# Optimization experiments

Measured on AMD Instinct MI355X. Metric: run time of the kernel, lower is better.

## Reference

```python
import jax, jax.numpy as jnp
import numpy as np

ALPHA = 0.2  # LeakyReLU negative slope
NEG = -1e12


def setup_inputs() -> dict:
    key = jax.random.key(0)
    ks = jax.random.split(key, 7)
    B, N, Cin, F, H = 4, 2048, 256, 64, 4
    x = jax.random.normal(ks[0], (B, N, Cin), dtype=jnp.float32)
    adj = jax.random.randint(ks[1], (N, N), 0, 2, dtype=jnp.int32)
    W = jax.random.normal(ks[2], (H, Cin, F), dtype=jnp.float32) * (1.414 / np.sqrt(Cin))
    a1 = jax.random.normal(ks[3], (H, F), dtype=jnp.float32) * 0.1
    a2 = jax.random.normal(ks[4], (H, F), dtype=jnp.float32) * 0.1
    Wl = jax.random.normal(ks[5], (F, H * F), dtype=jnp.float32) * (1.0 / np.sqrt(H * F))
    bl = jax.random.normal(ks[6], (F,), dtype=jnp.float32) * 0.01
    return {"x": x, "adj": adj, "W": W, "a1": a1, "a2": a2, "Wl": Wl, "bl": bl}


def leaky(v):
    return jnp.where(v >= 0, v, ALPHA * v)


def reference(x, adj, W, a1, a2, Wl, bl):
    # Eval mode: dropout is a no-op.
    # h: [B,H,N,F] per-head projected features
    h = jnp.einsum("bnc,hcf->bhnf", x, W)
    # additive attention: e[b,h,i,j] = leaky(h_i . a1 + h_j . a2)
    f1 = jnp.einsum("bhnf,hf->bhn", h, a1)  # source term
    f2 = jnp.einsum("bhnf,hf->bhn", h, a2)  # target term
    e = leaky(f1[:, :, :, None] + f2[:, :, None, :])  # [B,H,N,N]
    e = jnp.where(adj[None, None] > 0, e, NEG)
    # NOTE: original softmaxes over dim=1 of [B,N,N], i.e. the i axis (axis=2 here)
    att = jax.nn.softmax(e, axis=2)
    hp = jnp.einsum("bhij,bhjf->bhif", att, h)  # [B,H,N,F]
    hp = jax.nn.relu(hp)  # concat=True heads
    B, H, N, F = hp.shape
    cat = hp.transpose(0, 2, 1, 3).reshape(B, N, H * F)
    out = leaky(cat @ Wl.T + bl)  # n_heads > 1 -> linear + leakyrelu
    return out
```

## Files before the change

kernel.cpp:

```cpp
#include <hip/hip_runtime.h>
#include <hip/hip_bf16.h>
#include <stdint.h>

typedef __attribute__((ext_vector_type(8))) short short8;
typedef __attribute__((ext_vector_type(4))) float f32x4;
typedef uint32_t u32;
typedef uint16_t u16;
typedef uint8_t u8;

#define LOG2E 1.4426950408889634f


__device__ __forceinline__ u16 f2bf(float f){
  union{float f; u32 u;} x; x.f = f;
  u32 r = x.u + 0x7FFFu + ((x.u >> 16) & 1u);
  return (u16)(r >> 16);
}
__device__ __forceinline__ u32 pkbf(float a, float b){
  __hip_bfloat162 h = __float22bfloat162_rn(float2{a, b});
  union{ __hip_bfloat162 h; u32 u; } cv; cv.h = h;
  return cv.u;
}
__device__ __forceinline__ float bflo(u32 cd){ union{u32 u; float f;} v; v.u = cd << 16; return v.f; }
__device__ __forceinline__ float bfhi(u32 cd){ union{u32 u; float f;} v; v.u = cd & 0xFFFF0000u; return v.f; }

__global__ __launch_bounds__(256) void k_front(const float* __restrict__ x,
      const float* __restrict__ W, const float* __restrict__ a1, const float* __restrict__ a2,
      const int* __restrict__ adj,
      u8* __restrict__ adjb, u16* __restrict__ hT,
      float* __restrict__ Aarr, float* __restrict__ Barr,
      float* __restrict__ Cexp, float* __restrict__ Dexp,
      float* __restrict__ Dsum){
  int bid = blockIdx.x, t = threadIdx.x;

  if (bid >= 2560){
    Dsum[(bid - 2560)*256 + t] = 0.f;
    return;
  }
  if (bid >= 512){
    int idx = (bid - 512)*256 + t;
    const int4* ap = (const int4*)(adj + (size_t)idx*8);
    int4 v0 = ap[0], v1 = ap[1];
    u32 byte = (u32)(v0.x > 0)        | ((u32)(v0.y > 0) << 1)
             | ((u32)(v0.z > 0) << 2) | ((u32)(v0.w > 0) << 3)
             | ((u32)(v1.x > 0) << 4) | ((u32)(v1.y > 0) << 5)
             | ((u32)(v1.z > 0) << 6) | ((u32)(v1.w > 0) << 7);
    adjb[idx] = (u8)byte;
    return;
  }
  __shared__ u16 WL[64*264];
  int rt = bid & 127, cb = bid >> 7;
  const float* Wh = W + (size_t)cb*16384;
  #pragma unroll 4
  for (int p = 0; p < 16; p++){
    int idx = p*256 + t;
    float4 wv = ((const float4*)Wh)[idx];
    int off = idx*4; int c = off >> 6, f0 = off & 63;
    int cc = c ^ (((f0 >> 2) & 7) << 3);
    WL[(f0+0)*264 + cc] = f2bf(wv.x);
    WL[(f0+1)*264 + cc] = f2bf(wv.y);
    WL[(f0+2)*264 + cc] = f2bf(wv.z);
    WL[(f0+3)*264 + cc] = f2bf(wv.w);
  }
  __syncthreads();

  int w = t >> 6, l = t & 63;
  int rA = rt*64 + w*16 + (l & 15);
  int kg = (l >> 4) * 8;
  int rowq[4], rswq[4];
  #pragma unroll
  for (int q = 0; q < 4; q++){
    rowq[q] = q*16 + (l & 15);
    rswq[q] = ((rowq[q] >> 2) & 7) << 3;
  }
  f32x4 acc[4] = {};
  const float* xrow = x + (size_t)rA * 256;
  #pragma unroll
  for (int ks = 0; ks < 8; ks++){
    int c = ks*32 + kg;
    float4 xa = *(const float4*)(xrow + c);
    float4 xb = *(const float4*)(xrow + c + 4);
    union{u32 w[4]; short8 v;} A;
    A.w[0] = pkbf(xa.x, xa.y); A.w[1] = pkbf(xa.z, xa.w);
    A.w[2] = pkbf(xb.x, xb.y); A.w[3] = pkbf(xb.z, xb.w);
    #pragma unroll
    for (int q = 0; q < 4; q++){
      short8 Bf = *(const short8*)&WL[rowq[q]*264 + (c ^ rswq[q])];
      acc[q] = __builtin_amdgcn_mfma_f32_16x16x32_bf16(A.v, Bf, acc[q], 0, 0, 0);
    }
  }
  int rb = rt*64 + w*16 + (l >> 4)*4;
  int b = rb >> 11, n = rb & 2047;
  #pragma unroll
  for (int q = 0; q < 4; q++){
    int f = q*16 + (l & 15);
    u32 p0 = pkbf(acc[q][0], acc[q][1]);
    u32 p1 = pkbf(acc[q][2], acc[q][3]);
    u16* dst = hT + ((size_t)(b*4 + cb)*64 + f)*2048 + n;
    *(uint2*)dst = uint2{p0, p1};
  }
  float a1v[4], a2v[4];
  #pragma unroll
  for (int q = 0; q < 4; q++){
    a1v[q] = a1[cb*64 + q*16 + (l & 15)];
    a2v[q] = a2[cb*64 + q*16 + (l & 15)];
  }
  float s1[4], s2[4];
  #pragma unroll
  for (int r = 0; r < 4; r++){
    s1[r] = acc[0][r]*a1v[0] + acc[1][r]*a1v[1] + acc[2][r]*a1v[2] + acc[3][r]*a1v[3];
    s2[r] = acc[0][r]*a2v[0] + acc[1][r]*a2v[1] + acc[2][r]*a2v[2] + acc[3][r]*a2v[3];
  }
  #pragma unroll
  for (int m = 1; m <= 8; m <<= 1){
    #pragma unroll
    for (int r = 0; r < 4; r++){
      s1[r] += __shfl_xor(s1[r], m);
      s2[r] += __shfl_xor(s2[r], m);
    }
  }
  if ((l & 15) == 0){
    #pragma unroll
    for (int r = 0; r < 4; r++){
      int row = rb + r;
      int bb = row >> 11, nn = row & 2047;
      int o = (bb*4 + cb)*2048 + nn;
      float fa = s1[r] * LOG2E;
      Aarr[o] = __builtin_amdgcn_exp2f(fa);
      Barr[o] = __builtin_amdgcn_exp2f(0.2f*fa);
      float fb = s2[r] * LOG2E;
      Cexp[o] = __builtin_amdgcn_exp2f(fb);
      Dexp[o] = __builtin_amdgcn_exp2f(0.2f*fb);
    }
  }
}

__global__ __launch_bounds__(256) void k_colsum(const u32* __restrict__ adjw,
      const float* __restrict__ Aarr, const float* __restrict__ Barr,
      const float* __restrict__ Cexp, const float* __restrict__ Dexp,
      float* __restrict__ Dsum){
  __shared__ float AL[128*16], BL[128*16];
  __shared__ float red[4][1024];
  int jt = blockIdx.x;
  int is = blockIdx.y;
  int t = threadIdx.x, w = t >> 6, l = t & 63;
  int i0 = is*128;
  for (int k = t; k < 2048; k += 256){
    int bh = k >> 7, ii = k & 127;
    AL[ii*16 + bh] = Aarr[bh*2048 + i0 + ii];
    BL[ii*16 + bh] = Barr[bh*2048 + i0 + ii];
  }
  int j = jt*64 + l;
  float Cj[16], Dj[16];
  #pragma unroll
  for (int bh = 0; bh < 16; bh++){
    Cj[bh] = Cexp[bh*2048 + j];
    Dj[bh] = Dexp[bh*2048 + j];
  }
  float acc[16] = {};
  __syncthreads();
  int wi = jt*2 + (l >> 5), sh = l & 31;
  const u32* aw = adjw + wi;
  #pragma unroll 2
  for (int ii = w*32; ii < w*32 + 32; ii++){
    u32 m = aw[(size_t)(i0 + ii)*64];
    float bitf = (float)((m >> sh) & 1u);
    const float* ar = &AL[ii*16];
    const float* br = &BL[ii*16];
    #pragma unroll
    for (int q = 0; q < 4; q++){
      float4 a4 = *(const float4*)(ar + q*4);
      float4 b4 = *(const float4*)(br + q*4);
      acc[q*4+0] = fmaf(fmaxf(a4.x*Cj[q*4+0], b4.x*Dj[q*4+0]), bitf, acc[q*4+0]);
      acc[q*4+1] = fmaf(fmaxf(a4.y*Cj[q*4+1], b4.y*Dj[q*4+1]), bitf, acc[q*4+1]);
      acc[q*4+2] = fmaf(fmaxf(a4.z*Cj[q*4+2], b4.z*Dj[q*4+2]), bitf, acc[q*4+2]);
      acc[q*4+3] = fmaf(fmaxf(a4.w*Cj[q*4+3], b4.w*Dj[q*4+3]), bitf, acc[q*4+3]);
    }
  }
  #pragma unroll
  for (int bh = 0; bh < 16; bh++) red[w][bh*64 + l] = acc[bh];
  __syncthreads();
  #pragma unroll
  for (int k = 0; k < 4; k++){
    int e = t*4 + k;
    float s = (red[0][e] + red[1][e]) + (red[2][e] + red[3][e]);
    int bh = e >> 6, jl = e & 63;
    atomicAdd(&Dsum[bh*2048 + jt*64 + jl], s);
  }
}

__global__ __launch_bounds__(256) void k_pv(const u32* __restrict__ adjw, const u16* __restrict__ hT,
      const float* __restrict__ Aarr, const float* __restrict__ Barr,
      const float* __restrict__ Cexp, const float* __restrict__ Dexp,
      const float* __restrict__ Dsum, u16* __restrict__ part){
  int it = blockIdx.x;
  int bh = blockIdx.y;
  int jh = blockIdx.z;
  int b = bh >> 2, h = bh & 3;
  int t = threadIdx.x;
  int w = t >> 6, l = t & 63;

  __shared__ u16 hTl[64*136];
  __shared__ u32 CDl[1024];

  {
    int gj = bh*2048 + jh*1024 + t*4;
    float4 c4 = *(const float4*)(Cexp + gj);
    float4 d4 = *(const float4*)(Dexp + gj);
    float4 s4 = *(const float4*)(Dsum + gj);
    float i0v = 1.0f/s4.x, i1v = 1.0f/s4.y, i2v = 1.0f/s4.z, i3v = 1.0f/s4.w;
    uint4 pk;
    pk.x = pkbf(c4.x*i0v, d4.x*i0v);
    pk.y = pkbf(c4.y*i1v, d4.y*i1v);
    pk.z = pkbf(c4.z*i2v, d4.z*i2v);
    pk.w = pkbf(c4.w*i3v, d4.w*i3v);
    *(uint4*)&CDl[t*4] = pk;
  }

  int i0 = it*128 + w*32 + (l & 15);
  float Ai0 = Aarr[bh*2048 + i0],      Bi0 = Barr[bh*2048 + i0];
  float Ai1 = Aarr[bh*2048 + i0 + 16], Bi1 = Barr[bh*2048 + i0 + 16];
  const u16* hTr = hT + (size_t)bh * 64 * 2048;
  int kg = (l >> 4) * 8;
  f32x4 acc[2][4] = {};

  for (int jj = 0; jj < 1024; jj += 128){
    int jc = jh*1024 + jj;
    __syncthreads();
    {
      int f = t >> 2, seg = (t & 3) * 32;
      const u16* src = hTr + (size_t)f*2048 + jc + seg;
      u16* d = hTl + f*136 + seg;
      *(uint4*)(d)      = *(const uint4*)(src);
      *(uint4*)(d + 8)  = *(const uint4*)(src + 8);
      *(uint4*)(d + 16) = *(const uint4*)(src + 16);
      *(uint4*)(d + 24) = *(const uint4*)(src + 24);
    }
    __syncthreads();
    uint4 mw0 = *(const uint4*)(adjw + (size_t)i0*64 + (jc >> 5));
    uint4 mw1 = *(const uint4*)(adjw + (size_t)(i0+16)*64 + (jc >> 5));
    #pragma unroll
    for (int ks = 0; ks < 4; ks++){
      u32 cd[8];
      *(uint4*)(cd)     = *(const uint4*)&CDl[jj + ks*32 + kg];
      *(uint4*)(cd + 4) = *(const uint4*)&CDl[jj + ks*32 + kg + 4];
      u32 w0 = (&mw0.x)[ks] >> kg;
      u32 w1 = (&mw1.x)[ks] >> kg;
      float wv0[8], wv1[8];
      #pragma unroll
      for (int e = 0; e < 8; e++){
        float ca = bflo(cd[e]), db = bfhi(cd[e]);
        float ev0 = fmaxf(Ai0*ca, Bi0*db);
        float ev1 = fmaxf(Ai1*ca, Bi1*db);
        wv0[e] = ((int)(w0 << (31-e)) < 0) ? ev0 : 0.f;
        wv1[e] = ((int)(w1 << (31-e)) < 0) ? ev1 : 0.f;
      }
      union{u32 w[4]; short8 v;} A0, A1;
      A0.w[0] = pkbf(wv0[0], wv0[1]); A0.w[1] = pkbf(wv0[2], wv0[3]);
      A0.w[2] = pkbf(wv0[4], wv0[5]); A0.w[3] = pkbf(wv0[6], wv0[7]);
      A1.w[0] = pkbf(wv1[0], wv1[1]); A1.w[1] = pkbf(wv1[2], wv1[3]);
      A1.w[2] = pkbf(wv1[4], wv1[5]); A1.w[3] = pkbf(wv1[6], wv1[7]);
      #pragma unroll
      for (int q = 0; q < 4; q++){
        short8 Bf = *(const short8*)&hTl[(q*16 + (l & 15))*136 + ks*32 + kg];
        acc[0][q] = __builtin_amdgcn_mfma_f32_16x16x32_bf16(A0.v, Bf, acc[0][q], 0, 0, 0);
        acc[1][q] = __builtin_amdgcn_mfma_f32_16x16x32_bf16(A1.v, Bf, acc[1][q], 0, 0, 0);
      }
    }
  }
  u16* pr = part + ((size_t)(jh*4 + b)*2048)*256;
  #pragma unroll
  for (int r = 0; r < 2; r++){
    int nb = it*128 + w*32 + r*16 + (l >> 4)*4;
    #pragma unroll
    for (int q = 0; q < 4; q++){
      int f = h*64 + q*16 + (l & 15);
      #pragma unroll
      for (int rr = 0; rr < 4; rr++){
        pr[(size_t)(nb + rr)*256 + f] = f2bf(acc[r][q][rr]);
      }
    }
  }
}

__global__ __launch_bounds__(256) void k_out(const u16* __restrict__ part,
                       const float* __restrict__ Wl, const float* __restrict__ bl,
                       float* __restrict__ out){
  int rt = blockIdx.x;
  int w = threadIdx.x >> 6, l = threadIdx.x & 63;
  int rA = rt*64 + w*16 + (l & 15);
  int b = rA >> 11, n = rA & 2047;
  const u16* p0 = part + ((size_t)b*2048 + n)*256;
  const u16* p1 = part + ((size_t)(4 + b)*2048 + n)*256;
  int kg = (l >> 4) * 8;
  f32x4 acc[4] = {};
  #pragma unroll
  for (int ks = 0; ks < 8; ks++){
    int c = ks*32 + kg;
    short8 v0 = *(const short8*)(p0 + c);
    short8 v1 = *(const short8*)(p1 + c);
    float av[8];
    #pragma unroll
    for (int e = 0; e < 8; e++){
      union{u32 u; float f;} x0, x1;
      x0.u = ((u32)(u16)v0[e]) << 16;
      x1.u = ((u32)(u16)v1[e]) << 16;
      av[e] = fmaxf(x0.f + x1.f, 0.f);
    }
    union{u32 w[4]; short8 v;} A;
    A.w[0] = pkbf(av[0], av[1]); A.w[1] = pkbf(av[2], av[3]);
    A.w[2] = pkbf(av[4], av[5]); A.w[3] = pkbf(av[6], av[7]);
    #pragma unroll
    for (int q = 0; q < 4; q++){
      const float* wr = Wl + (size_t)(q*16 + (l & 15))*256 + c;
      float4 u0 = *(const float4*)(wr);
      float4 u1 = *(const float4*)(wr + 4);
      union{u32 w[4]; short8 v;} Bv;
      Bv.w[0] = pkbf(u0.x, u0.y); Bv.w[1] = pkbf(u0.z, u0.w);
      Bv.w[2] = pkbf(u1.x, u1.y); Bv.w[3] = pkbf(u1.z, u1.w);
      acc[q] = __builtin_amdgcn_mfma_f32_16x16x32_bf16(A.v, Bv.v, acc[q], 0, 0, 0);
    }
  }
  int rb = rt*64 + w*16 + (l >> 4)*4;
  #pragma unroll
  for (int q = 0; q < 4; q++){
    int o = q*16 + (l & 15);
    float bv = bl[o];
    #pragma unroll
    for (int r = 0; r < 4; r++){
      float v = acc[q][r] + bv;
      out[(size_t)(rb + r)*64 + o] = fmaxf(v, 0.2f*v);
    }
  }
}

extern "C" void kernel_launch(void* const* d_in, const int* in_sizes, int n_in,
                              void* d_out, int out_size, void* d_ws, size_t ws_size,
                              hipStream_t stream) {
  const float* x  = (const float*)d_in[0];
  const int* adj  = (const int*)d_in[1];
  const float* W  = (const float*)d_in[2];
  const float* a1 = (const float*)d_in[3];
  const float* a2 = (const float*)d_in[4];
  const float* Wl = (const float*)d_in[5];
  const float* bl = (const float*)d_in[6];
  float* out = (float*)d_out;
  char* ws = (char*)d_ws;

  u32* adjw    = (u32*)(ws + 0x0000000);
  u16* hT      = (u16*)(ws + 0x0080000);
  u16* part    = (u16*)(ws + 0x0480000);
  float* Aarr  = (float*)(ws + 0x1480000);
  float* Barr  = (float*)(ws + 0x14A0000);
  float* Cexp  = (float*)(ws + 0x14C0000);
  float* Dexp  = (float*)(ws + 0x14E0000);
  float* Dsum  = (float*)(ws + 0x1500000);

  k_front<<<2688, 256, 0, stream>>>(x, W, a1, a2, adj, (u8*)adjw, hT, Aarr, Barr, Cexp, Dexp, Dsum);
  k_colsum<<<dim3(32, 16), 256, 0, stream>>>(adjw, Aarr, Barr, Cexp, Dexp, Dsum);
  k_pv<<<dim3(16, 16, 2), 256, 0, stream>>>(adjw, hT, Aarr, Barr, Cexp, Dexp, Dsum, part);
  k_out<<<128, 256, 0, stream>>>(part, Wl, bl, out);
}
```

Measured before the change: 71.31 us.

## Switch attention P·V path to packed fp16 math and fp16 MFMA

Stores the per-head projected features in fp16 instead of bf16. The P·V kernel now builds attention weights with packed half2 multiply/max and bitmask AND, replacing per-element fp32 math and bf16 packing, and feeds fp16 MFMA. Scale factors of 16 and 1/16 keep the values inside fp16 range. Separately, the W staging in the front kernel is rewritten to use coalesced row loads with packed 64-bit LDS stores. The trade is fewer VALU ops per weight against fp16 range and overflow risk for the exp-based terms.

```diff
diff --git a/kernel.cpp b/kernel.cpp
--- a/kernel.cpp
+++ b/kernel.cpp
@@ -4,6 +4,9 @@
 
 typedef __attribute__((ext_vector_type(8))) short short8;
 typedef __attribute__((ext_vector_type(4))) float f32x4;
+typedef _Float16 f16;
+typedef __attribute__((ext_vector_type(8))) f16 f16x8;
+typedef __attribute__((ext_vector_type(2))) f16 f16x2;
 typedef uint32_t u32;
 typedef uint16_t u16;
 typedef uint8_t u8;
@@ -21,8 +24,13 @@
   union{ __hip_bfloat162 h; u32 u; } cv; cv.h = h;
   return cv.u;
 }
-__device__ __forceinline__ float bflo(u32 cd){ union{u32 u; float f;} v; v.u = cd << 16; return v.f; }
-__device__ __forceinline__ float bfhi(u32 cd){ union{u32 u; float f;} v; v.u = cd & 0xFFFF0000u; return v.f; }
+__device__ __forceinline__ u32 pkh(float a, float b){
+  f16x2 h; h.x = (f16)a; h.y = (f16)b;
+  union{ f16x2 h; u32 u; } cv; cv.h = h;
+  return cv.u;
+}
+__device__ __forceinline__ f16x2 uh2(u32 x){ union{u32 u; f16x2 h;} v; v.u = x; return v.h; }
+__device__ __forceinline__ u32 h2u(f16x2 x){ union{f16x2 h; u32 u;} v; v.h = x; return v.u; }
 
 __global__ __launch_bounds__(256) void k_front(const float* __restrict__ x,
       const float* __restrict__ W, const float* __restrict__ a1, const float* __restrict__ a2,
@@ -51,16 +59,25 @@
   __shared__ u16 WL[64*264];
   int rt = bid & 127, cb = bid >> 7;
   const float* Wh = W + (size_t)cb*16384;
-  #pragma unroll 4
-  for (int p = 0; p < 16; p++){
-    int idx = p*256 + t;
-    float4 wv = ((const float4*)Wh)[idx];
-    int off = idx*4; int c = off >> 6, f0 = off & 63;
-    int cc = c ^ (((f0 >> 2) & 7) << 3);
-    WL[(f0+0)*264 + cc] = f2bf(wv.x);
-    WL[(f0+1)*264 + cc] = f2bf(wv.y);
-    WL[(f0+2)*264 + cc] = f2bf(wv.z);
-    WL[(f0+3)*264 + cc] = f2bf(wv.w);
+  {
+    int f0 = (t & 15)*4;
+    int cg = t >> 4;
+    int s = ((f0 >> 2) & 7) << 3;
+    #pragma unroll
+    for (int it2 = 0; it2 < 4; it2++){
+      int c0 = (cg + it2*16)*4;
+      float4 wv0 = *(const float4*)(Wh + (size_t)(c0+0)*64 + f0);
+      float4 wv1 = *(const float4*)(Wh + (size_t)(c0+1)*64 + f0);
+      float4 wv2 = *(const float4*)(Wh + (size_t)(c0+2)*64 + f0);
+      float4 wv3 = *(const float4*)(Wh + (size_t)(c0+3)*64 + f0);
+      int cc = c0 ^ s;
+      #pragma unroll
+      for (int k = 0; k < 4; k++){
+        u32 lo = pkbf((&wv0.x)[k], (&wv1.x)[k]);
+        u32 hi = pkbf((&wv2.x)[k], (&wv3.x)[k]);
+        *(uint2*)&WL[(f0+k)*264 + cc] = uint2{lo, hi};
+      }
+    }
   }
   __syncthreads();
 
@@ -94,8 +111,8 @@
   #pragma unroll
   for (int q = 0; q < 4; q++){
     int f = q*16 + (l & 15);
-    u32 p0 = pkbf(acc[q][0], acc[q][1]);
-    u32 p1 = pkbf(acc[q][2], acc[q][3]);
+    u32 p0 = pkh(acc[q][0], acc[q][1]);
+    u32 p1 = pkh(acc[q][2], acc[q][3]);
     u16* dst = hT + ((size_t)(b*4 + cb)*64 + f)*2048 + n;
     *(uint2*)dst = uint2{p0, p1};
   }
@@ -201,25 +218,30 @@
   int w = t >> 6, l = t & 63;
 
   __shared__ u16 hTl[64*136];
-  __shared__ u32 CDl[1024];
+  __shared__ u32 CA2l[512];
+  __shared__ u32 DB2l[512];
 
   {
     int gj = bh*2048 + jh*1024 + t*4;
     float4 c4 = *(const float4*)(Cexp + gj);
     float4 d4 = *(const float4*)(Dexp + gj);
     float4 s4 = *(const float4*)(Dsum + gj);
-    float i0v = 1.0f/s4.x, i1v = 1.0f/s4.y, i2v = 1.0f/s4.z, i3v = 1.0f/s4.w;
-    uint4 pk;
-    pk.x = pkbf(c4.x*i0v, d4.x*i0v);
-    pk.y = pkbf(c4.y*i1v, d4.y*i1v);
-    pk.z = pkbf(c4.z*i2v, d4.z*i2v);
-    pk.w = pkbf(c4.w*i3v, d4.w*i3v);
-    *(uint4*)&CDl[t*4] = pk;
+    float i0v = 16.0f/s4.x, i1v = 16.0f/s4.y, i2v = 16.0f/s4.z, i3v = 16.0f/s4.w;
+    CA2l[t*2]   = pkh(c4.x*i0v, c4.y*i1v);
+    CA2l[t*2+1] = pkh(c4.z*i2v, c4.w*i3v);
+    DB2l[t*2]   = pkh(d4.x*i0v, d4.y*i1v);
+    DB2l[t*2+1] = pkh(d4.z*i2v, d4.w*i3v);
   }
 
   int i0 = it*128 + w*32 + (l & 15);
-  float Ai0 = Aarr[bh*2048 + i0],      Bi0 = Barr[bh*2048 + i0];
-  float Ai1 = Aarr[bh*2048 + i0 + 16], Bi1 = Barr[bh*2048 + i0 + 16];
+  f16x2 Ai02, Bi02, Ai12, Bi12;
+  {
+    const float sc = 0.0625f;
+    float A0 = Aarr[bh*2048 + i0] * sc,      B0 = Barr[bh*2048 + i0] * sc;
+    float A1 = Aarr[bh*2048 + i0 + 16] * sc, B1 = Barr[bh*2048 + i0 + 16] * sc;
+    Ai02 = uh2(pkh(A0, A0)); Bi02 = uh2(pkh(B0, B0));
+    Ai12 = uh2(pkh(A1, A1)); Bi12 = uh2(pkh(B1, B1));
+  }
   const u16* hTr = hT + (size_t)bh * 64 * 2048;
   int kg = (l >> 4) * 8;
   f32x4 acc[2][4] = {};
@@ -241,30 +263,30 @@
     uint4 mw1 = *(const uint4*)(adjw + (size_t)(i0+16)*64 + (jc >> 5));
     #pragma unroll
     for (int ks = 0; ks < 4; ks++){
-      u32 cd[8];
-      *(uint4*)(cd)     = *(const uint4*)&CDl[jj + ks*32 + kg];
-      *(uint4*)(cd + 4) = *(const uint4*)&CDl[jj + ks*32 + kg + 4];
+      int pbase = (jj >> 1) + ks*16 + (l >> 4)*4;
+      uint4 ca2 = *(const uint4*)&CA2l[pbase];
+      uint4 db2 = *(const uint4*)&DB2l[pbase];
       u32 w0 = (&mw0.x)[ks] >> kg;
       u32 w1 = (&mw1.x)[ks] >> kg;
-      float wv0[8], wv1[8];
+      union{u32 w[4]; f16x8 v;} A0u, A1u;
       #pragma unroll
-      for (int e = 0; e < 8; e++){
-        float ca = bflo(cd[e]), db = bfhi(cd[e]);
-        float ev0 = fmaxf(Ai0*ca, Bi0*db);
-        float ev1 = fmaxf(Ai1*ca, Bi1*db);
-        wv0[e] = ((int)(w0 << (31-e)) < 0) ? ev0 : 0.f;
-        wv1[e] = ((int)(w1 << (31-e)) < 0) ? ev1 : 0.f;
+      for (int p = 0; p < 4; p++){
+        f16x2 cav = uh2((&ca2.x)[p]);
+        f16x2 dbv = uh2((&db2.x)[p]);
+        f16x2 e0 = __builtin_elementwise_max(Ai02*cav, Bi02*dbv);
+        f16x2 e1 = __builtin_elementwise_max(Ai12*cav, Bi12*dbv);
+        u32 m0 = ((u32)((int)(w0 << (31-2*p)) >> 31) & 0x0000FFFFu)
+               | ((u32)((int)(w0 << (30-2*p)) >> 31) & 0xFFFF0000u);
+        u32 m1 = ((u32)((int)(w1 << (31-2*p)) >> 31) & 0x0000FFFFu)
+               | ((u32)((int)(w1 << (30-2*p)) >> 31) & 0xFFFF0000u);
+        A0u.w[p] = h2u(e0) & m0;
+        A1u.w[p] = h2u(e1) & m1;
       }
-      union{u32 w[4]; short8 v;} A0, A1;
-      A0.w[0] = pkbf(wv0[0], wv0[1]); A0.w[1] = pkbf(wv0[2], wv0[3]);
-      A0.w[2] = pkbf(wv0[4], wv0[5]); A0.w[3] = pkbf(wv0[6], wv0[7]);
-      A1.w[0] = pkbf(wv1[0], wv1[1]); A1.w[1] = pkbf(wv1[2], wv1[3]);
-      A1.w[2] = pkbf(wv1[4], wv1[5]); A1.w[3] = pkbf(wv1[6], wv1[7]);
       #pragma unroll
       for (int q = 0; q < 4; q++){
-        short8 Bf = *(const short8*)&hTl[(q*16 + (l & 15))*136 + ks*32 + kg];
-        acc[0][q] = __builtin_amdgcn_mfma_f32_16x16x32_bf16(A0.v, Bf, acc[0][q], 0, 0, 0);
-        acc[1][q] = __builtin_amdgcn_mfma_f32_16x16x32_bf16(A1.v, Bf, acc[1][q], 0, 0, 0);
+        f16x8 Bf = *(const f16x8*)&hTl[(q*16 + (l & 15))*136 + ks*32 + kg];
+        acc[0][q] = __builtin_amdgcn_mfma_f32_16x16x32_f16(A0u.v, Bf, acc[0][q], 0, 0, 0);
+        acc[1][q] = __builtin_amdgcn_mfma_f32_16x16x32_f16(A1u.v, Bf, acc[1][q], 0, 0, 0);
       }
     }
   }
```

After: 70.02 us. No clear change (-1.8%).
